# Kernel tuning notes

Measured on AMD Instinct MI355X. Metric: run time of the kernel, lower is better.

Reference implementation:

```python
import jax, jax.numpy as jnp
import numpy as np

B, C, H, W = 4, 1, 240, 320
M_BINS = 256


def setup_inputs() -> dict:
    key = jax.random.key(0)
    k1, k2 = jax.random.split(key)
    # positive depth-like values; max per image is > 0 so division is safe
    target = jax.random.uniform(k1, (B, C, H, W), dtype=jnp.float32) + 1e-3
    bin_centers = jax.random.uniform(k2, (B, M_BINS), dtype=jnp.float32)
    return {"target": target, "bin_centers": bin_centers}


def reference(target, bin_centers):
    # scale-invariant normalization: divide by per-image max (mask=None path)
    target_max = jnp.amax(target, axis=(2, 3), keepdims=True)        # [B, C, 1, 1]
    target_n = target / target_max                                   # [B, C, H, W]
    bin_centers_n = bin_centers / target_max[:, :, 0, 0]             # [B, M] (C==1)

    t = target_n.reshape(target_n.shape[0], -1)                      # [B, N] flattened pixels
    b = bin_centers_n                                                # [B, M]
    N = t.shape[1]
    M = b.shape[1]

    # pairwise squared differences [B, M, N]
    sq = (b[:, :, None] - t[:, None, :]) ** 2

    # bins -> nearest pixel: amin over N, sum over M, normalized by M
    d_b2t = jnp.sum(jnp.amin(sq, axis=2), axis=1) / M                # [B]
    # pixels -> nearest bin: amin over M, sum over N, normalized by N
    d_t2b = jnp.sum(jnp.amin(sq, axis=1), axis=1) / N                # [B]

    loss = jnp.sum(d_b2t + d_t2b) / t.shape[0] * 10.0
    return loss.reshape(1)  # original returns a shape-[1] tensor
```

## Files before the change

### kernel.cpp

```cpp
#include <hip/hip_runtime.h>

namespace {
constexpr int B_ = 4;
constexpr int N_ = 240 * 320;
constexpr int M_ = 256;
constexpr int TILE = 512;
constexpr int CHUNKS = N_ / TILE;
constexpr int TILES = B_ * CHUNKS;
constexpr int NBLK = 2 * TILES;
constexpr float BIG = 3.0e38f;

constexpr int WS_BINMIN = 0;
constexpr int WS_T2B = B_ * M_;
constexpr int WS_MAX = WS_T2B + TILES;
}

__device__ __forceinline__ void pmin4(float& acc, const float4 c, const float t) {
  float d0 = c.x - t; d0 *= d0;
  float d1 = c.y - t; d1 *= d1;
  float d2 = c.z - t; d2 *= d2;
  float d3 = c.w - t; d3 *= d3;
  float x = fminf(fminf(d0, d1), d2);
  acc = fminf(fminf(x, d3), acc);
}

__global__ __launch_bounds__(128) void chamfer_main_kernel(const float* __restrict__ target,
                                                           const float* __restrict__ bins,
                                                           unsigned* __restrict__ wsu) {
  float* wsf = reinterpret_cast<float*>(wsu);
  const int bid = blockIdx.x;
  const int role = bid & 1;
  const int tile = bid >> 1;
  const int b = tile / CHUNKS;
  const int chunk = tile - b * CHUNKS;
  const int tid = threadIdx.x;

  __shared__ __align__(16) float lds[TILE];
  __shared__ float red2[4];

  const float4 px =
      reinterpret_cast<const float4*>(target + b * N_ + chunk * TILE)[tid];

  if (role == 0) {
    reinterpret_cast<float2*>(lds)[tid] =
        reinterpret_cast<const float2*>(bins + b * M_)[tid];
    __syncthreads();
    const float4* bins4 = reinterpret_cast<const float4*>(lds);
    float a0 = BIG, a1 = BIG, a2 = BIG, a3 = BIG;
#pragma unroll 4
    for (int m4 = 0; m4 < M_ / 4; ++m4) {
      const float4 c = bins4[m4];
      pmin4(a0, c, px.x);
      pmin4(a1, c, px.y);
      pmin4(a2, c, px.z);
      pmin4(a3, c, px.w);
    }
    float s = (a0 + a1) + (a2 + a3);
    float mx = fmaxf(fmaxf(px.x, px.y), fmaxf(px.z, px.w));
#pragma unroll
    for (int o = 32; o > 0; o >>= 1) {
      s += __shfl_down(s, o);
      mx = fmaxf(mx, __shfl_down(mx, o));
    }
    if ((tid & 63) == 0) {
      red2[tid >> 6] = s;
      red2[2 + (tid >> 6)] = mx;
    }
    __syncthreads();
    if (tid == 0) {
      wsf[WS_T2B + tile] = red2[0] + red2[1];
      wsf[WS_MAX + tile] = fmaxf(red2[2], red2[3]);
    }
  } else {
    reinterpret_cast<float4*>(lds)[tid] = px;
    const int g = tid & 63;
    const int h = tid >> 6;
    const float4 cj = reinterpret_cast<const float4*>(bins + b * M_)[g];
    __syncthreads();
    const float4* t4 = reinterpret_cast<const float4*>(lds) + h * 64;
    float b0 = BIG, b1 = BIG, b2 = BIG, b3 = BIG;
#pragma unroll 4
    for (int p4 = 0; p4 < 64; ++p4) {
      const float4 u = t4[p4];
      pmin4(b0, u, cj.x);
      pmin4(b1, u, cj.y);
      pmin4(b2, u, cj.z);
      pmin4(b3, u, cj.w);
    }
    __syncthreads();
    reinterpret_cast<float4*>(lds)[h * 64 + g] = make_float4(b0, b1, b2, b3);
    __syncthreads();
    const float2 f0 = reinterpret_cast<const float2*>(lds)[tid];
    const float2 f1 = reinterpret_cast<const float2*>(lds)[128 + tid];
    atomicMin(&wsu[WS_BINMIN + b * M_ + 2 * tid],
              __float_as_uint(fminf(f0.x, f1.x)));
    atomicMin(&wsu[WS_BINMIN + b * M_ + 2 * tid + 1],
              __float_as_uint(fminf(f0.y, f1.y)));
  }
}

__global__ __launch_bounds__(1024) void chamfer_final_kernel(const unsigned* __restrict__ wsu,
                                                             float* __restrict__ out) {
  const float* wsf = reinterpret_cast<const float*>(wsu);
  const int tid = threadIdx.x;
  const int bb = tid >> 8;
  const int k = tid & 255;

  float sb = __uint_as_float(wsu[WS_BINMIN + bb * M_ + k]);
  float st = (k < CHUNKS) ? wsf[WS_T2B + bb * CHUNKS + k] : 0.f;
  float sm = (k < CHUNKS) ? wsf[WS_MAX + bb * CHUNKS + k] : 0.f;
#pragma unroll
  for (int o = 32; o > 0; o >>= 1) {
    sb += __shfl_down(sb, o);
    st += __shfl_down(st, o);
    sm = fmaxf(sm, __shfl_down(sm, o));
  }
  __shared__ float l_sb[16], l_st[16], l_sm[16];
  if ((tid & 63) == 0) {
    const int w = tid >> 6;
    l_sb[w] = sb; l_st[w] = st; l_sm[w] = sm;
  }
  __syncthreads();
  if (tid == 0) {
    float loss = 0.f;
#pragma unroll
    for (int b2 = 0; b2 < B_; ++b2) {
      float s1 = 0.f, s2 = 0.f, m = 0.f;
#pragma unroll
      for (int w = 0; w < 4; ++w) {
        s1 += l_sb[b2 * 4 + w];
        s2 += l_st[b2 * 4 + w];
        m = fmaxf(m, l_sm[b2 * 4 + w]);
      }
      const float inv = 1.0f / (m * m);
      loss += (s1 / (float)M_) * inv + (s2 / (float)N_) * inv;
    }
    out[0] = loss / (float)B_ * 10.0f;
  }
}

extern "C" void kernel_launch(void* const* d_in, const int* in_sizes, int n_in,
                              void* d_out, int out_size, void* d_ws, size_t ws_size,
                              hipStream_t stream) {
  (void)in_sizes; (void)n_in; (void)out_size; (void)ws_size;
  const float* target = reinterpret_cast<const float*>(d_in[0]);
  const float* bins = reinterpret_cast<const float*>(d_in[1]);
  unsigned* ws = reinterpret_cast<unsigned*>(d_ws);
  float* out = reinterpret_cast<float*>(d_out);

  chamfer_main_kernel<<<NBLK, 128, 0, stream>>>(target, bins, ws);
  chamfer_final_kernel<<<1, 1024, 0, stream>>>(ws, out);
}
```

Before: 20.89 us.

## Replace brute-force pairwise min with sorted bins and binary search

Each block ranks the 256 bin centers to sort them in shared memory, then each pixel finds its nearest bin by binary search instead of scanning all bins. Bin-to-pixel distances are recovered by recording the min and max pixel value falling in each sorted interval, merged globally via atomics. A prefix-max/suffix-min scan in the final kernel then gives each bin its nearest pixel. This removes the O(N·M) work but adds per-block sorting, shared atomics, and reliance on a specific workspace fill value.

```diff
diff --git a/kernel.cpp b/kernel.cpp
--- a/kernel.cpp
+++ b/kernel.cpp
@@ -4,99 +4,109 @@
 constexpr int B_ = 4;
 constexpr int N_ = 240 * 320;
 constexpr int M_ = 256;
-constexpr int TILE = 512;
-constexpr int CHUNKS = N_ / TILE;
-constexpr int TILES = B_ * CHUNKS;
-constexpr int NBLK = 2 * TILES;
+constexpr int PXB = 1024;
+constexpr int CHUNKS = N_ / PXB;
+constexpr int NBLK = B_ * CHUNKS;
 constexpr float BIG = 3.0e38f;
-
-constexpr int WS_BINMIN = 0;
-constexpr int WS_T2B = B_ * M_;
-constexpr int WS_MAX = WS_T2B + TILES;
-}
-
-__device__ __forceinline__ void pmin4(float& acc, const float4 c, const float t) {
-  float d0 = c.x - t; d0 *= d0;
-  float d1 = c.y - t; d1 *= d1;
-  float d2 = c.z - t; d2 *= d2;
-  float d3 = c.w - t; d3 *= d3;
-  float x = fminf(fminf(d0, d1), d2);
-  acc = fminf(fminf(x, d3), acc);
-}
-
-__global__ __launch_bounds__(128) void chamfer_main_kernel(const float* __restrict__ target,
-                                                           const float* __restrict__ bins,
-                                                           unsigned* __restrict__ wsu) {
+constexpr unsigned POISON = 0xAAAAAAAAu;
+
+constexpr int WS_GMIN = 0;
+constexpr int WS_GMAX = B_ * (M_ + 1);
+constexpr int WS_SORT = 2 * B_ * (M_ + 1);
+constexpr int WS_T2B = WS_SORT + B_ * M_;
+constexpr int WS_MAXP = WS_T2B + NBLK;
+}
+
+__global__ __launch_bounds__(512) void chamfer_px_kernel(const float* __restrict__ target,
+                                                         const float* __restrict__ bins,
+                                                         unsigned* __restrict__ wsu) {
   float* wsf = reinterpret_cast<float*>(wsu);
   const int bid = blockIdx.x;
-  const int role = bid & 1;
-  const int tile = bid >> 1;
-  const int b = tile / CHUNKS;
-  const int chunk = tile - b * CHUNKS;
+  const int b = bid / CHUNKS;
+  const int chunk = bid - b * CHUNKS;
   const int tid = threadIdx.x;
 
-  __shared__ __align__(16) float lds[TILE];
-  __shared__ float red2[4];
-
-  const float4 px =
-      reinterpret_cast<const float4*>(target + b * N_ + chunk * TILE)[tid];
-
-  if (role == 0) {
-    reinterpret_cast<float2*>(lds)[tid] =
-        reinterpret_cast<const float2*>(bins + b * M_)[tid];
-    __syncthreads();
-    const float4* bins4 = reinterpret_cast<const float4*>(lds);
-    float a0 = BIG, a1 = BIG, a2 = BIG, a3 = BIG;
+  __shared__ __align__(16) float raw[M_];
+  __shared__ float sbin[M_];
+  __shared__ unsigned imin[M_ + 1], imax[M_ + 1];
+  __shared__ float red[16];
+
+  if (tid < M_) raw[tid] = bins[b * M_ + tid];
+  for (int i = tid; i < M_ + 1; i += 512) {
+    imin[i] = 0x7f800000u;
+    imax[i] = 0u;
+  }
+  __syncthreads();
+
+  if (tid < M_) {
+    const float myv = raw[tid];
+    int rank = 0;
+    const float4* r4 = reinterpret_cast<const float4*>(raw);
 #pragma unroll 4
-    for (int m4 = 0; m4 < M_ / 4; ++m4) {
-      const float4 c = bins4[m4];
-      pmin4(a0, c, px.x);
-      pmin4(a1, c, px.y);
-      pmin4(a2, c, px.z);
-      pmin4(a3, c, px.w);
-    }
-    float s = (a0 + a1) + (a2 + a3);
-    float mx = fmaxf(fmaxf(px.x, px.y), fmaxf(px.z, px.w));
-#pragma unroll
-    for (int o = 32; o > 0; o >>= 1) {
-      s += __shfl_down(s, o);
-      mx = fmaxf(mx, __shfl_down(mx, o));
-    }
-    if ((tid & 63) == 0) {
-      red2[tid >> 6] = s;
-      red2[2 + (tid >> 6)] = mx;
-    }
-    __syncthreads();
-    if (tid == 0) {
-      wsf[WS_T2B + tile] = red2[0] + red2[1];
-      wsf[WS_MAX + tile] = fmaxf(red2[2], red2[3]);
-    }
-  } else {
-    reinterpret_cast<float4*>(lds)[tid] = px;
-    const int g = tid & 63;
-    const int h = tid >> 6;
-    const float4 cj = reinterpret_cast<const float4*>(bins + b * M_)[g];
-    __syncthreads();
-    const float4* t4 = reinterpret_cast<const float4*>(lds) + h * 64;
-    float b0 = BIG, b1 = BIG, b2 = BIG, b3 = BIG;
-#pragma unroll 4
-    for (int p4 = 0; p4 < 64; ++p4) {
-      const float4 u = t4[p4];
-      pmin4(b0, u, cj.x);
-      pmin4(b1, u, cj.y);
-      pmin4(b2, u, cj.z);
-      pmin4(b3, u, cj.w);
-    }
-    __syncthreads();
-    reinterpret_cast<float4*>(lds)[h * 64 + g] = make_float4(b0, b1, b2, b3);
-    __syncthreads();
-    const float2 f0 = reinterpret_cast<const float2*>(lds)[tid];
-    const float2 f1 = reinterpret_cast<const float2*>(lds)[128 + tid];
-    atomicMin(&wsu[WS_BINMIN + b * M_ + 2 * tid],
-              __float_as_uint(fminf(f0.x, f1.x)));
-    atomicMin(&wsu[WS_BINMIN + b * M_ + 2 * tid + 1],
-              __float_as_uint(fminf(f0.y, f1.y)));
-  }
+    for (int k4 = 0; k4 < M_ / 4; ++k4) {
+      const float4 v = r4[k4];
+      const int k = k4 * 4;
+      rank += (v.x < myv || (v.x == myv && k + 0 < tid)) ? 1 : 0;
+      rank += (v.y < myv || (v.y == myv && k + 1 < tid)) ? 1 : 0;
+      rank += (v.z < myv || (v.z == myv && k + 2 < tid)) ? 1 : 0;
+      rank += (v.w < myv || (v.w == myv && k + 3 < tid)) ? 1 : 0;
+    }
+    sbin[rank] = myv;
+  }
+  __syncthreads();
+
+  const float2 px =
+      reinterpret_cast<const float2*>(target + b * N_ + chunk * PXB)[tid];
+
+  float ssum = 0.f;
+#pragma unroll
+  for (int e = 0; e < 2; ++e) {
+    const float t = (e == 0) ? px.x : px.y;
+    int pos = 0;
+#pragma unroll
+    for (int step = 128; step > 0; step >>= 1)
+      if (sbin[pos + step - 1] <= t) pos += step;
+    if (pos < M_ && sbin[pos] <= t) ++pos;
+    float dl = BIG, dr = BIG;
+    if (pos > 0)  { const float d = t - sbin[pos - 1]; dl = d * d; }
+    if (pos < M_) { const float d = sbin[pos] - t;     dr = d * d; }
+    ssum += fminf(dl, dr);
+    atomicMin(&imin[pos], __float_as_uint(t));
+    atomicMax(&imax[pos], __float_as_uint(t));
+  }
+
+  float mx = fmaxf(px.x, px.y);
+#pragma unroll
+  for (int o = 32; o > 0; o >>= 1) {
+    ssum += __shfl_down(ssum, o);
+    mx = fmaxf(mx, __shfl_down(mx, o));
+  }
+  if ((tid & 63) == 0) {
+    red[tid >> 6] = ssum;
+    red[8 + (tid >> 6)] = mx;
+  }
+  __syncthreads();
+
+  if (tid == 0) {
+    float s = 0.f, m = 0.f;
+#pragma unroll
+    for (int w = 0; w < 8; ++w) {
+      s += red[w];
+      m = fmaxf(m, red[8 + w]);
+    }
+    wsf[WS_T2B + bid] = s;
+    wsf[WS_MAXP + bid] = m;
+  }
+
+  for (int i = tid; i < M_ + 1; i += 512) {
+    const unsigned mn = imin[i];
+    if (mn != 0x7f800000u) atomicMin(&wsu[WS_GMIN + b * (M_ + 1) + i], mn);
+    const unsigned mb = imax[i];
+    if (mb != 0u)
+      atomicMax(&wsu[WS_GMAX + b * (M_ + 1) + i],
+                __float_as_uint(-__uint_as_float(mb)));
+  }
+  if (chunk == 0 && tid < M_) wsf[WS_SORT + b * M_ + tid] = sbin[tid];
 }
 
 __global__ __launch_bounds__(1024) void chamfer_final_kernel(const unsigned* __restrict__ wsu,
@@ -104,23 +114,60 @@
   const float* wsf = reinterpret_cast<const float*>(wsu);
   const int tid = threadIdx.x;
   const int bb = tid >> 8;
-  const int k = tid & 255;
-
-  float sb = __uint_as_float(wsu[WS_BINMIN + bb * M_ + k]);
-  float st = (k < CHUNKS) ? wsf[WS_T2B + bb * CHUNKS + k] : 0.f;
-  float sm = (k < CHUNKS) ? wsf[WS_MAX + bb * CHUNKS + k] : 0.f;
+  const int j = tid & 255;
+
+  __shared__ float pm[B_][M_ + 8];
+  __shared__ float sm[B_][M_ + 8];
+  __shared__ float red[48];
+
+  {
+    const unsigned u = wsu[WS_GMAX + bb * (M_ + 1) + j];
+    pm[bb][j] = (u == POISON) ? -BIG : -__uint_as_float(u);
+    const unsigned v = wsu[WS_GMIN + bb * (M_ + 1) + j];
+    sm[bb][j] = (v == POISON) ? BIG : __uint_as_float(v);
+    if (j == 255) {
+      const unsigned u6 = wsu[WS_GMAX + bb * (M_ + 1) + 256];
+      pm[bb][256] = (u6 == POISON) ? -BIG : -__uint_as_float(u6);
+      const unsigned v6 = wsu[WS_GMIN + bb * (M_ + 1) + 256];
+      sm[bb][256] = (v6 == POISON) ? BIG : __uint_as_float(v6);
+    }
+  }
+  const float c = wsf[WS_SORT + bb * M_ + j];
+  __syncthreads();
+
+  for (int off = 1; off <= 256; off <<= 1) {
+    const float p_own = pm[bb][j];
+    const float p_nb = (j >= off) ? pm[bb][j - off] : -BIG;
+    const float s_own = sm[bb][j];
+    const float s_nb = (j + off <= 256) ? sm[bb][j + off] : BIG;
+    __syncthreads();
+    pm[bb][j] = fmaxf(p_own, p_nb);
+    sm[bb][j] = fminf(s_own, s_nb);
+    __syncthreads();
+  }
+
+  const float below = pm[bb][j];
+  const float above = sm[bb][j + 1];
+  const float d1 = (below == -BIG) ? BIG : (c - below) * (c - below);
+  const float d2 = (above == BIG) ? BIG : (above - c) * (above - c);
+  float vb = fminf(d1, d2);
+
+  float st = (j < CHUNKS) ? wsf[WS_T2B + bb * CHUNKS + j] : 0.f;
+  float sx = (j < CHUNKS) ? wsf[WS_MAXP + bb * CHUNKS + j] : 0.f;
 #pragma unroll
   for (int o = 32; o > 0; o >>= 1) {
-    sb += __shfl_down(sb, o);
+    vb += __shfl_down(vb, o);
     st += __shfl_down(st, o);
-    sm = fmaxf(sm, __shfl_down(sm, o));
-  }
-  __shared__ float l_sb[16], l_st[16], l_sm[16];
+    sx = fmaxf(sx, __shfl_down(sx, o));
+  }
   if ((tid & 63) == 0) {
     const int w = tid >> 6;
-    l_sb[w] = sb; l_st[w] = st; l_sm[w] = sm;
-  }
-  __syncthreads();
+    red[w] = vb;
+    red[16 + w] = st;
+    red[32 + w] = sx;
+  }
+  __syncthreads();
+
   if (tid == 0) {
     float loss = 0.f;
 #pragma unroll
@@ -128,9 +175,9 @@
       float s1 = 0.f, s2 = 0.f, m = 0.f;
 #pragma unroll
       for (int w = 0; w < 4; ++w) {
-        s1 += l_sb[b2 * 4 + w];
-        s2 += l_st[b2 * 4 + w];
-        m = fmaxf(m, l_sm[b2 * 4 + w]);
+        s1 += red[b2 * 4 + w];
+        s2 += red[16 + b2 * 4 + w];
+        m = fmaxf(m, red[32 + b2 * 4 + w]);
       }
       const float inv = 1.0f / (m * m);
       loss += (s1 / (float)M_) * inv + (s2 / (float)N_) * inv;
@@ -148,6 +195,6 @@
   unsigned* ws = reinterpret_cast<unsigned*>(d_ws);
   float* out = reinterpret_cast<float*>(d_out);
 
-  chamfer_main_kernel<<<NBLK, 128, 0, stream>>>(target, bins, ws);
+  chamfer_px_kernel<<<NBLK, 512, 0, stream>>>(target, bins, ws);
   chamfer_final_kernel<<<1, 1024, 0, stream>>>(ws, out);
 }
```

After: 22.49 us. 1.08x slower.
